# Kernel optimization log

Measured on AMD Instinct MI355X. Metric: run time of the kernel, lower is better.

## Reference

```python
import jax, jax.numpy as jnp
import numpy as np

B, T, D = 4, 1024, 1024       # batch, tokens, emb_size
E, K, F_EXP = 8, 2, 1024      # num_expert, num_expert_active, expert_size
NUM_BLOCK = 12


def setup_inputs() -> dict:
    key = jax.random.key(0)
    k_x, k_b, k_r, k_1, k_2 = jax.random.split(key, 5)
    x = jax.random.normal(k_x, (B, T, D), dtype=jnp.float32)
    auxfree_bias = jax.random.normal(k_b, (E,), dtype=jnp.float32) * 0.1
    router_w = jax.random.normal(k_r, (E, D), dtype=jnp.float32) * 0.02
    # GroupedLinear weight{i}: [out_features, in_features], applied as x @ W^T
    w1 = jax.random.normal(k_1, (E, F_EXP, D), dtype=jnp.float32) * 0.02
    w2 = jax.random.normal(k_2, (E, D, F_EXP), dtype=jnp.float32) * (0.02 / np.sqrt(2.0 * NUM_BLOCK))
    return {"x": x, "auxfree_bias": auxfree_bias, "router_w": router_w, "w1": w1, "w2": w2}


def reference(x, auxfree_bias, router_w, w1, w2):
    # --- routing: top-k on bias-adjusted DETACHED logits, gather raw logits ---
    logits = jnp.einsum("btd,ed->bte", x, router_w)              # [B,T,E]
    biased = jax.lax.stop_gradient(logits) + auxfree_bias        # bias only affects selection
    _, idx = jax.lax.top_k(biased, K)                            # [B,T,K] int32
    gathered = jnp.take_along_axis(logits, idx, axis=-1)         # [B,T,K]
    probs = jax.nn.softmax(gathered, axis=-1)                    # [B,T,K]

    # combine weights per expert: sum_k probs_k * 1[idx_k == e]  -> [B,T,E]
    combine = jnp.sum(jax.nn.one_hot(idx, E, dtype=x.dtype) * probs[..., None], axis=2)

    # --- experts: out = sum_e combine_e * (gelu(x W1_e^T) W2_e^T) ---
    # (dense per-expert reference for the dispatch -> grouped GEMM -> combine pipeline;
    #  tokens with combine weight 0 contribute nothing, matching the sparse original)
    out = jnp.zeros_like(x)
    for e in range(E):
        h = jax.nn.gelu(jnp.einsum("btd,fd->btf", x, w1[e]), approximate=False)
        out = out + combine[:, :, e:e + 1] * jnp.einsum("btf,df->btd", h, w2[e])
    return out
```

## Files before the change

### kernel.cpp

```cpp
#include <hip/hip_runtime.h>
#include <hip/hip_bf16.h>

#define D_DIM 1024
#define F_DIM 1024
#define NTOK  4096
#define NEXP  8
#define CAP   4096

typedef __attribute__((ext_vector_type(8))) short bf16x8;
typedef __attribute__((ext_vector_type(4))) float f32x4;
typedef __attribute__((ext_vector_type(8))) unsigned short u16x8;

__device__ __forceinline__ unsigned short f2bf(float f) {
    unsigned int u = __float_as_uint(f);
    u = u + 0x7fffu + ((u >> 16) & 1u);
    return (unsigned short)(u >> 16);
}

__device__ __forceinline__ void async_copy16(void* lds, const void* gsrc) {
    __builtin_amdgcn_global_load_lds(
        (const __attribute__((address_space(1))) unsigned int*)gsrc,
        (__attribute__((address_space(3))) unsigned int*)lds, 16, 0, 0);
}

__global__ __launch_bounds__(256) void cvt_kernel(const float* __restrict__ in,
                                                  unsigned short* __restrict__ out, int n) {
    int i = (blockIdx.x * 256 + threadIdx.x) * 8;
    if (i >= n) return;
    const float4* p = (const float4*)(in + i);
    float4 a = p[0], b = p[1];
    u16x8 r;
    r[0] = f2bf(a.x); r[1] = f2bf(a.y); r[2] = f2bf(a.z); r[3] = f2bf(a.w);
    r[4] = f2bf(b.x); r[5] = f2bf(b.y); r[6] = f2bf(b.z); r[7] = f2bf(b.w);
    *(u16x8*)(out + i) = r;
}

__global__ __launch_bounds__(256) void logits_kernel(
    const float* __restrict__ x, const float* __restrict__ rw,
    float* __restrict__ logits)
{
    const int wave = threadIdx.x >> 6, lane = threadIdx.x & 63;
    const int t = blockIdx.x * 4 + wave;
    double s[NEXP];
    #pragma unroll
    for (int e = 0; e < NEXP; ++e) s[e] = 0.0;
    const float* xp = x + (size_t)t * D_DIM;
    for (int kk = 0; kk < D_DIM; kk += 64) {
        float xv = xp[kk + lane];
        #pragma unroll
        for (int e = 0; e < NEXP; ++e)
            s[e] += (double)xv * (double)rw[e * D_DIM + kk + lane];
    }
    #pragma unroll
    for (int e = 0; e < NEXP; ++e) {
        double v = s[e];
        for (int off = 32; off; off >>= 1) v += __shfl_xor(v, off, 64);
        s[e] = v;
    }
    if (lane == 0) {
        #pragma unroll
        for (int e = 0; e < NEXP; ++e) logits[(size_t)t * NEXP + e] = (float)s[e];
    }
}

__global__ __launch_bounds__(256) void assign_kernel(
    const float* __restrict__ logits, const float* __restrict__ bias,
    int* counts, int* list, float* wlist)
{
    __shared__ int lcnt[NEXP];
    __shared__ int lbase[NEXP];
    const int tid = threadIdx.x;
    const int t = blockIdx.x * 256 + tid;
    if (tid < NEXP) lcnt[tid] = 0;
    __syncthreads();

    float lg[NEXP], b2[NEXP];
    #pragma unroll
    for (int e = 0; e < NEXP; ++e) {
        lg[e] = logits[(size_t)t * NEXP + e];
        b2[e] = lg[e] + bias[e];
    }
    int i0 = 0; float b0v = b2[0], l0v = lg[0];
    #pragma unroll
    for (int e = 1; e < NEXP; ++e)
        if (b2[e] > b0v) { b0v = b2[e]; l0v = lg[e]; i0 = e; }
    int i1 = -1; float b1v = 0.f, l1v = 0.f;
    #pragma unroll
    for (int e = 0; e < NEXP; ++e) {
        if (e == i0) continue;
        bool take = (i1 < 0) || (b2[e] > b1v);
        if (take) { i1 = e; b1v = b2[e]; l1v = lg[e]; }
    }
    float m = fmaxf(l0v, l1v);
    float e0 = expf(l0v - m), e1 = expf(l1v - m);
    float inv = 1.0f / (e0 + e1);

    int lp0 = atomicAdd(&lcnt[i0], 1);
    int lp1 = atomicAdd(&lcnt[i1], 1);
    __syncthreads();
    if (tid < NEXP) lbase[tid] = atomicAdd(&counts[tid], lcnt[tid]);
    __syncthreads();

    int p0 = lbase[i0] + lp0;
    list[i0 * CAP + p0] = t; wlist[i0 * CAP + p0] = e0 * inv;
    int p1 = lbase[i1] + lp1;
    list[i1 * CAP + p1] = t; wlist[i1 * CAP + p1] = e1 * inv;
}

__global__ void scan_kernel(const int* __restrict__ counts, int* __restrict__ offs) {
    if (threadIdx.x == 0) {
        int a = 0;
        for (int e = 0; e < NEXP; ++e) { offs[e] = a; a += counts[e]; }
        offs[NEXP] = a;
    }
}

#define STAGE(AB, BB, k0)                                                   \
    do {                                                                    \
        _Pragma("unroll")                                                   \
        for (int i = 0; i < 4; ++i) {                                       \
            async_copy16(&AB[(wave * 4 + i) * 512], ap[i] + (k0));          \
            async_copy16(&BB[(wave * 4 + i) * 512], bp_[i] + (k0));         \
        }                                                                   \
    } while (0)

#define COMPUTE(AB, BB)                                                     \
    do {                                                                    \
        _Pragma("unroll")                                                   \
        for (int kk = 0; kk < 2; ++kk) {                                    \
            bf16x8 af[4], bfv[4];                                           \
            const int sbase = kk * 4 + (lane >> 4);                         \
            const int phys  = (sbase ^ (lane & 7)) * 8;                     \
            _Pragma("unroll")                                               \
            for (int m = 0; m < 4; ++m)                                     \
                af[m] = *(const bf16x8*)&AB[(wr * 64 + m * 16 + (lane & 15)) * 64 + phys]; \
            _Pragma("unroll")                                               \
            for (int n = 0; n < 4; ++n)                                     \
                bfv[n] = *(const bf16x8*)&BB[(wc * 64 + n * 16 + (lane & 15)) * 64 + phys]; \
            _Pragma("unroll")                                               \
            for (int m = 0; m < 4; ++m)                                     \
                _Pragma("unroll")                                           \
                for (int n = 0; n < 4; ++n)                                 \
                    acc[m][n] = __builtin_amdgcn_mfma_f32_16x16x32_bf16(af[m], bfv[n], acc[m][n], 0, 0, 0); \
        }                                                                   \
    } while (0)

__global__ __launch_bounds__(256) void gemm1_kernel(
    const unsigned short* __restrict__ xb,
    const unsigned short* __restrict__ w1b,
    const int* __restrict__ counts, const int* __restrict__ offs,
    const int* __restrict__ list,
    unsigned short* __restrict__ H)
{
    const int e  = blockIdx.y >> 5;
    const int rb = blockIdx.y & 31;
    const int ne = counts[e];
    if (rb * 128 >= ne) return;
    const int row0 = rb * 128;
    const int n0 = blockIdx.x * 128;
    const int hbase = offs[e];

    __shared__ __align__(16) unsigned short As0[128 * 64], As1[128 * 64];
    __shared__ __align__(16) unsigned short Bs0[128 * 64], Bs1[128 * 64];
    __shared__ int toks[128];

    const int tid = threadIdx.x;
    if (tid < 128) {
        int i = row0 + tid;
        if (i >= ne) i = ne - 1;
        toks[tid] = list[e * CAP + i];
    }
    __syncthreads();

    const int wave = tid >> 6, lane = tid & 63;
    const int wr = wave >> 1, wc = wave & 1;

    const int lr  = lane >> 3;
    const int swz = ((lane & 7) ^ lr) * 8;
    const unsigned short* ap[4];
    const unsigned short* bp_[4];
    const unsigned short* wbase = w1b + (size_t)e * F_DIM * D_DIM;
    #pragma unroll
    for (int i = 0; i < 4; ++i) {
        int r = wave * 32 + i * 8 + lr;
        ap[i]  = xb + (size_t)toks[r] * D_DIM + swz;
        bp_[i] = wbase + (size_t)(n0 + r) * D_DIM + swz;
    }

    f32x4 acc[4][4];
    #pragma unroll
    for (int m = 0; m < 4; ++m)
        #pragma unroll
        for (int n = 0; n < 4; ++n) acc[m][n] = (f32x4){0.f, 0.f, 0.f, 0.f};

    STAGE(As0, Bs0, 0);
    __syncthreads();
    for (int t = 0; t < 7; ++t) {
        STAGE(As1, Bs1, t * 128 + 64);
        COMPUTE(As0, Bs0);
        __syncthreads();
        STAGE(As0, Bs0, t * 128 + 128);
        COMPUTE(As1, Bs1);
        __syncthreads();
    }
    STAGE(As1, Bs1, 960);
    COMPUTE(As0, Bs0);
    __syncthreads();
    COMPUTE(As1, Bs1);

    #pragma unroll
    for (int m = 0; m < 4; ++m) {
        #pragma unroll
        for (int j = 0; j < 4; ++j) {
            int ri = wr * 64 + m * 16 + (lane >> 4) * 4 + j;
            int i = row0 + ri;
            if (i < ne) {
                unsigned short* hp = H + (size_t)(hbase + i) * F_DIM + n0 + wc * 64;
                #pragma unroll
                for (int n = 0; n < 4; ++n) {
                    float v = acc[m][n][j];
                    float g = 0.5f * v * (1.0f + erff(v * 0.70710678118654752f));
                    hp[n * 16 + (lane & 15)] = f2bf(g);
                }
            }
        }
    }
}

__global__ __launch_bounds__(256) void gemm2_kernel(
    const unsigned short* __restrict__ H,
    const unsigned short* __restrict__ w2b,
    const int* __restrict__ counts, const int* __restrict__ offs,
    const int* __restrict__ list, const float* __restrict__ wlist,
    float* __restrict__ out)
{
    const int e  = blockIdx.y >> 5;
    const int rb = blockIdx.y & 31;
    const int ne = counts[e];
    if (rb * 128 >= ne) return;
    const int row0 = rb * 128;
    const int n0 = blockIdx.x * 128;
    const int hbase = offs[e];

    __shared__ __align__(16) unsigned short As0[128 * 64], As1[128 * 64];
    __shared__ __align__(16) unsigned short Bs0[128 * 64], Bs1[128 * 64];
    __shared__ int toks[128];
    __shared__ float wts[128];

    const int tid = threadIdx.x;
    if (tid < 128) {
        int i = row0 + tid;
        if (i >= ne) i = ne - 1;
        toks[tid] = list[e * CAP + i];
        wts[tid]  = wlist[e * CAP + i];
    }
    __syncthreads();

    const int wave = tid >> 6, lane = tid & 63;
    const int wr = wave >> 1, wc = wave & 1;

    const int lr  = lane >> 3;
    const int swz = ((lane & 7) ^ lr) * 8;
    const unsigned short* ap[4];
    const unsigned short* bp_[4];
    const unsigned short* wbase = w2b + (size_t)e * D_DIM * F_DIM;
    #pragma unroll
    for (int i = 0; i < 4; ++i) {
        int r = wave * 32 + i * 8 + lr;
        ap[i]  = H + (size_t)(hbase + row0 + r) * F_DIM + swz;
        bp_[i] = wbase + (size_t)(n0 + r) * F_DIM + swz;
    }

    f32x4 acc[4][4];
    #pragma unroll
    for (int m = 0; m < 4; ++m)
        #pragma unroll
        for (int n = 0; n < 4; ++n) acc[m][n] = (f32x4){0.f, 0.f, 0.f, 0.f};

    STAGE(As0, Bs0, 0);
    __syncthreads();
    for (int t = 0; t < 7; ++t) {
        STAGE(As1, Bs1, t * 128 + 64);
        COMPUTE(As0, Bs0);
        __syncthreads();
        STAGE(As0, Bs0, t * 128 + 128);
        COMPUTE(As1, Bs1);
        __syncthreads();
    }
    STAGE(As1, Bs1, 960);
    COMPUTE(As0, Bs0);
    __syncthreads();
    COMPUTE(As1, Bs1);

    #pragma unroll
    for (int m = 0; m < 4; ++m) {
        #pragma unroll
        for (int j = 0; j < 4; ++j) {
            int ri = wr * 64 + m * 16 + (lane >> 4) * 4 + j;
            int i = row0 + ri;
            if (i < ne) {
                int t = toks[ri];
                float wt = wts[ri];
                float* op = out + (size_t)t * D_DIM + n0 + wc * 64;
                #pragma unroll
                for (int n = 0; n < 4; ++n)
                    atomicAdd(&op[n * 16 + (lane & 15)], wt * acc[m][n][j]);
            }
        }
    }
}

extern "C" void kernel_launch(void* const* d_in, const int* in_sizes, int n_in,
                              void* d_out, int out_size, void* d_ws, size_t ws_size,
                              hipStream_t stream)
{
    const float* x    = (const float*)d_in[0];
    const float* bias = (const float*)d_in[1];
    const float* rw   = (const float*)d_in[2];
    const float* w1   = (const float*)d_in[3];
    const float* w2   = (const float*)d_in[4];
    float* out = (float*)d_out;

    char* ws = (char*)d_ws;
    size_t cur = 0;
    auto alloc = [&](size_t bytes) -> void* {
        void* p = (void*)(ws + cur);
        cur += (bytes + 255) & ~(size_t)255;
        return p;
    };
    unsigned short* xb   = (unsigned short*)alloc((size_t)NTOK * D_DIM * 2);
    unsigned short* w1b  = (unsigned short*)alloc((size_t)NEXP * F_DIM * D_DIM * 2);
    unsigned short* w2b  = (unsigned short*)alloc((size_t)NEXP * F_DIM * D_DIM * 2);
    unsigned short* Hb   = (unsigned short*)alloc((size_t)(NTOK * 2 + 128) * F_DIM * 2);
    float* logits = (float*)alloc((size_t)NTOK * NEXP * 4);
    int*   list   = (int*)alloc(NEXP * CAP * 4);
    float* wlist  = (float*)alloc(NEXP * CAP * 4);
    int*   counts = (int*)alloc(64);
    int*   offs   = (int*)alloc(64);

    hipMemsetAsync(counts, 0, 64, stream);
    hipMemsetAsync(out, 0, (size_t)out_size * 4, stream);

    cvt_kernel<<<NTOK * D_DIM / 2048, 256, 0, stream>>>(x, xb, NTOK * D_DIM);
    cvt_kernel<<<NEXP * F_DIM * D_DIM / 2048, 256, 0, stream>>>(w1, w1b, NEXP * F_DIM * D_DIM);
    cvt_kernel<<<NEXP * F_DIM * D_DIM / 2048, 256, 0, stream>>>(w2, w2b, NEXP * F_DIM * D_DIM);
    logits_kernel<<<NTOK / 4, 256, 0, stream>>>(x, rw, logits);
    assign_kernel<<<NTOK / 256, 256, 0, stream>>>(logits, bias, counts, list, wlist);
    scan_kernel<<<1, 64, 0, stream>>>(counts, offs);
    gemm1_kernel<<<dim3(8, 256), 256, 0, stream>>>(xb, w1b, counts, offs, list, Hb);
    gemm2_kernel<<<dim3(8, 256), 256, 0, stream>>>(Hb, w2b, counts, offs, list, wlist, out);
}
```

Measured before the change: 251.3 us.

## Shrink GEMM N-tile to 64, drop LDS double buffering, inline expert offset scan

Both grouped GEMMs now use 128x64 output tiles with a single LDS buffer and a simple load-sync-compute-sync loop, doubling the grid in the N dimension. The separate scan kernel is removed; each block computes its expert's row offset by summing counts directly. The smaller tile and smaller LDS footprint are meant to raise occupancy and block count, and removing the scan saves one launch. In exchange, arithmetic intensity per tile drops, the A-tile (gathered tokens) is re-read twice as often, and global loads no longer overlap with MFMA work.

```diff
diff --git a/kernel.cpp b/kernel.cpp
--- a/kernel.cpp
+++ b/kernel.cpp
@@ -107,40 +107,32 @@
     list[i1 * CAP + p1] = t; wlist[i1 * CAP + p1] = e1 * inv;
 }
 
-__global__ void scan_kernel(const int* __restrict__ counts, int* __restrict__ offs) {
-    if (threadIdx.x == 0) {
-        int a = 0;
-        for (int e = 0; e < NEXP; ++e) { offs[e] = a; a += counts[e]; }
-        offs[NEXP] = a;
-    }
-}
-
 #define STAGE(AB, BB, k0)                                                   \
     do {                                                                    \
         _Pragma("unroll")                                                   \
-        for (int i = 0; i < 4; ++i) {                                       \
+        for (int i = 0; i < 4; ++i)                                         \
             async_copy16(&AB[(wave * 4 + i) * 512], ap[i] + (k0));          \
-            async_copy16(&BB[(wave * 4 + i) * 512], bp_[i] + (k0));         \
-        }                                                                   \
+        _Pragma("unroll")                                                   \
+        for (int i = 0; i < 2; ++i)                                         \
+            async_copy16(&BB[(wave * 2 + i) * 512], bp_[i] + (k0));         \
     } while (0)
 
 #define COMPUTE(AB, BB)                                                     \
     do {                                                                    \
         _Pragma("unroll")                                                   \
         for (int kk = 0; kk < 2; ++kk) {                                    \
-            bf16x8 af[4], bfv[4];                                           \
-            const int sbase = kk * 4 + (lane >> 4);                         \
-            const int phys  = (sbase ^ (lane & 7)) * 8;                     \
+            bf16x8 af[4], bfv[2];                                           \
+            const int phys = (((kk * 4) + (lane >> 4)) ^ (lane & 7)) * 8;   \
             _Pragma("unroll")                                               \
             for (int m = 0; m < 4; ++m)                                     \
                 af[m] = *(const bf16x8*)&AB[(wr * 64 + m * 16 + (lane & 15)) * 64 + phys]; \
             _Pragma("unroll")                                               \
-            for (int n = 0; n < 4; ++n)                                     \
-                bfv[n] = *(const bf16x8*)&BB[(wc * 64 + n * 16 + (lane & 15)) * 64 + phys]; \
+            for (int n = 0; n < 2; ++n)                                     \
+                bfv[n] = *(const bf16x8*)&BB[(wc * 32 + n * 16 + (lane & 15)) * 64 + phys]; \
             _Pragma("unroll")                                               \
             for (int m = 0; m < 4; ++m)                                     \
                 _Pragma("unroll")                                           \
-                for (int n = 0; n < 4; ++n)                                 \
+                for (int n = 0; n < 2; ++n)                                 \
                     acc[m][n] = __builtin_amdgcn_mfma_f32_16x16x32_bf16(af[m], bfv[n], acc[m][n], 0, 0, 0); \
         }                                                                   \
     } while (0)
@@ -148,7 +140,7 @@
 __global__ __launch_bounds__(256) void gemm1_kernel(
     const unsigned short* __restrict__ xb,
     const unsigned short* __restrict__ w1b,
-    const int* __restrict__ counts, const int* __restrict__ offs,
+    const int* __restrict__ counts,
     const int* __restrict__ list,
     unsigned short* __restrict__ H)
 {
@@ -157,11 +149,13 @@
     const int ne = counts[e];
     if (rb * 128 >= ne) return;
     const int row0 = rb * 128;
-    const int n0 = blockIdx.x * 128;
-    const int hbase = offs[e];
-
-    __shared__ __align__(16) unsigned short As0[128 * 64], As1[128 * 64];
-    __shared__ __align__(16) unsigned short Bs0[128 * 64], Bs1[128 * 64];
+    const int n0 = blockIdx.x * 64;
+    int hbase = 0;
+    #pragma unroll
+    for (int ee = 0; ee < NEXP; ++ee) if (ee < e) hbase += counts[ee];
+
+    __shared__ __align__(16) unsigned short As[128 * 64];
+    __shared__ __align__(16) unsigned short Bs[64 * 64];
     __shared__ int toks[128];
 
     const int tid = threadIdx.x;
@@ -178,35 +172,27 @@
     const int lr  = lane >> 3;
     const int swz = ((lane & 7) ^ lr) * 8;
     const unsigned short* ap[4];
-    const unsigned short* bp_[4];
+    const unsigned short* bp_[2];
     const unsigned short* wbase = w1b + (size_t)e * F_DIM * D_DIM;
     #pragma unroll
-    for (int i = 0; i < 4; ++i) {
-        int r = wave * 32 + i * 8 + lr;
-        ap[i]  = xb + (size_t)toks[r] * D_DIM + swz;
-        bp_[i] = wbase + (size_t)(n0 + r) * D_DIM + swz;
-    }
-
-    f32x4 acc[4][4];
+    for (int i = 0; i < 4; ++i)
+        ap[i] = xb + (size_t)toks[wave * 32 + i * 8 + lr] * D_DIM + swz;
+    #pragma unroll
+    for (int i = 0; i < 2; ++i)
+        bp_[i] = wbase + (size_t)(n0 + wave * 16 + i * 8 + lr) * D_DIM + swz;
+
+    f32x4 acc[4][2];
     #pragma unroll
     for (int m = 0; m < 4; ++m)
         #pragma unroll
-        for (int n = 0; n < 4; ++n) acc[m][n] = (f32x4){0.f, 0.f, 0.f, 0.f};
-
-    STAGE(As0, Bs0, 0);
-    __syncthreads();
-    for (int t = 0; t < 7; ++t) {
-        STAGE(As1, Bs1, t * 128 + 64);
-        COMPUTE(As0, Bs0);
+        for (int n = 0; n < 2; ++n) acc[m][n] = (f32x4){0.f, 0.f, 0.f, 0.f};
+
+    for (int k0 = 0; k0 < D_DIM; k0 += 64) {
+        STAGE(As, Bs, k0);
         __syncthreads();
-        STAGE(As0, Bs0, t * 128 + 128);
-        COMPUTE(As1, Bs1);
+        COMPUTE(As, Bs);
         __syncthreads();
     }
-    STAGE(As1, Bs1, 960);
-    COMPUTE(As0, Bs0);
-    __syncthreads();
-    COMPUTE(As1, Bs1);
 
     #pragma unroll
     for (int m = 0; m < 4; ++m) {
@@ -215,9 +201,9 @@
             int ri = wr * 64 + m * 16 + (lane >> 4) * 4 + j;
             int i = row0 + ri;
             if (i < ne) {
-                unsigned short* hp = H + (size_t)(hbase + i) * F_DIM + n0 + wc * 64;
+                unsigned short* hp = H + (size_t)(hbase + i) * F_DIM + n0 + wc * 32;
                 #pragma unroll
-                for (int n = 0; n < 4; ++n) {
+                for (int n = 0; n < 2; ++n) {
                     float v = acc[m][n][j];
                     float g = 0.5f * v * (1.0f + erff(v * 0.70710678118654752f));
                     hp[n * 16 + (lane & 15)] = f2bf(g);
@@ -230,7 +216,7 @@
 __global__ __launch_bounds__(256) void gemm2_kernel(
     const unsigned short* __restrict__ H,
     const unsigned short* __restrict__ w2b,
-    const int* __restrict__ counts, const int* __restrict__ offs,
+    const int* __restrict__ counts,
     const int* __restrict__ list, const float* __restrict__ wlist,
     float* __restrict__ out)
 {
@@ -239,11 +225,13 @@
     const int ne = counts[e];
     if (rb * 128 >= ne) return;
     const int row0 = rb * 128;
-    const int n0 = blockIdx.x * 128;
-    const int hbase = offs[e];
-
-    __shared__ __align__(16) unsigned short As0[128 * 64], As1[128 * 64];
-    __shared__ __align__(16) unsigned short Bs0[128 * 64], Bs1[128 * 64];
+    const int n0 = blockIdx.x * 64;
+    int hbase = 0;
+    #pragma unroll
+    for (int ee = 0; ee < NEXP; ++ee) if (ee < e) hbase += counts[ee];
+
+    __shared__ __align__(16) unsigned short As[128 * 64];
+    __shared__ __align__(16) unsigned short Bs[64 * 64];
     __shared__ int toks[128];
     __shared__ float wts[128];
 
@@ -262,35 +250,27 @@
     const int lr  = lane >> 3;
     const int swz = ((lane & 7) ^ lr) * 8;
     const unsigned short* ap[4];
-    const unsigned short* bp_[4];
+    const unsigned short* bp_[2];
     const unsigned short* wbase = w2b + (size_t)e * D_DIM * F_DIM;
     #pragma unroll
-    for (int i = 0; i < 4; ++i) {
-        int r = wave * 32 + i * 8 + lr;
-        ap[i]  = H + (size_t)(hbase + row0 + r) * F_DIM + swz;
-        bp_[i] = wbase + (size_t)(n0 + r) * F_DIM + swz;
-    }
-
-    f32x4 acc[4][4];
+    for (int i = 0; i < 4; ++i)
+        ap[i] = H + (size_t)(hbase + row0 + wave * 32 + i * 8 + lr) * F_DIM + swz;
+    #pragma unroll
+    for (int i = 0; i < 2; ++i)
+        bp_[i] = wbase + (size_t)(n0 + wave * 16 + i * 8 + lr) * F_DIM + swz;
+
+    f32x4 acc[4][2];
     #pragma unroll
     for (int m = 0; m < 4; ++m)
         #pragma unroll
-        for (int n = 0; n < 4; ++n) acc[m][n] = (f32x4){0.f, 0.f, 0.f, 0.f};
-
-    STAGE(As0, Bs0, 0);
-    __syncthreads();
-    for (int t = 0; t < 7; ++t) {
-        STAGE(As1, Bs1, t * 128 + 64);
-        COMPUTE(As0, Bs0);
+        for (int n = 0; n < 2; ++n) acc[m][n] = (f32x4){0.f, 0.f, 0.f, 0.f};
+
+    for (int k0 = 0; k0 < F_DIM; k0 += 64) {
+        STAGE(As, Bs, k0);
         __syncthreads();
-        STAGE(As0, Bs0, t * 128 + 128);
-        COMPUTE(As1, Bs1);
+        COMPUTE(As, Bs);
         __syncthreads();
     }
-    STAGE(As1, Bs1, 960);
-    COMPUTE(As0, Bs0);
-    __syncthreads();
-    COMPUTE(As1, Bs1);
 
     #pragma unroll
     for (int m = 0; m < 4; ++m) {
@@ -301,9 +281,9 @@
             if (i < ne) {
                 int t = toks[ri];
                 float wt = wts[ri];
-                float* op = out + (size_t)t * D_DIM + n0 + wc * 64;
+                float* op = out + (size_t)t * D_DIM + n0 + wc * 32;
                 #pragma unroll
-                for (int n = 0; n < 4; ++n)
+                for (int n = 0; n < 2; ++n)
                     atomicAdd(&op[n * 16 + (lane & 15)], wt * acc[m][n][j]);
             }
         }
@@ -336,7 +316,6 @@
     int*   list   = (int*)alloc(NEXP * CAP * 4);
     float* wlist  = (float*)alloc(NEXP * CAP * 4);
     int*   counts = (int*)alloc(64);
-    int*   offs   = (int*)alloc(64);
 
     hipMemsetAsync(counts, 0, 64, stream);
     hipMemsetAsync(out, 0, (size_t)out_size * 4, stream);
@@ -346,7 +325,6 @@
     cvt_kernel<<<NEXP * F_DIM * D_DIM / 2048, 256, 0, stream>>>(w2, w2b, NEXP * F_DIM * D_DIM);
     logits_kernel<<<NTOK / 4, 256, 0, stream>>>(x, rw, logits);
     assign_kernel<<<NTOK / 256, 256, 0, stream>>>(logits, bias, counts, list, wlist);
-    scan_kernel<<<1, 64, 0, stream>>>(counts, offs);
-    gemm1_kernel<<<dim3(8, 256), 256, 0, stream>>>(xb, w1b, counts, offs, list, Hb);
-    gemm2_kernel<<<dim3(8, 256), 256, 0, stream>>>(Hb, w2b, counts, offs, list, wlist, out);
-}
+    gemm1_kernel<<<dim3(16, 256), 256, 0, stream>>>(xb, w1b, counts, list, Hb);
+    gemm2_kernel<<<dim3(16, 256), 256, 0, stream>>>(Hb, w2b, counts, list, wlist, out);
+}
```

New measurement: 236.5 us. -5.9%, faster.

## Deepen GEMM K-loop prefetch with vmcnt waits and drop scan kernel

Applied to the files above, without the earlier changes.

Replaces the double-buffered K loop in both grouped GEMMs with a fully unrolled loop that keeps two stages in flight. It uses explicit s_waitcnt vmcnt and raw s_barrier instead of __syncthreads, so the async LDS loads for the next tile overlap with compute on the current one. It also removes the single-thread scan kernel launch and computes each expert's row offset inline from the counts. The manual vmcnt counting depends on the exact number of outstanding loads per stage, so a miscount could race.

```diff
diff --git a/kernel.cpp b/kernel.cpp
--- a/kernel.cpp
+++ b/kernel.cpp
@@ -107,14 +107,6 @@
     list[i1 * CAP + p1] = t; wlist[i1 * CAP + p1] = e1 * inv;
 }
 
-__global__ void scan_kernel(const int* __restrict__ counts, int* __restrict__ offs) {
-    if (threadIdx.x == 0) {
-        int a = 0;
-        for (int e = 0; e < NEXP; ++e) { offs[e] = a; a += counts[e]; }
-        offs[NEXP] = a;
-    }
-}
-
 #define STAGE(AB, BB, k0)                                                   \
     do {                                                                    \
         _Pragma("unroll")                                                   \
@@ -129,8 +121,7 @@
         _Pragma("unroll")                                                   \
         for (int kk = 0; kk < 2; ++kk) {                                    \
             bf16x8 af[4], bfv[4];                                           \
-            const int sbase = kk * 4 + (lane >> 4);                         \
-            const int phys  = (sbase ^ (lane & 7)) * 8;                     \
+            const int phys = (((kk * 4) + (lane >> 4)) ^ (lane & 7)) * 8;   \
             _Pragma("unroll")                                               \
             for (int m = 0; m < 4; ++m)                                     \
                 af[m] = *(const bf16x8*)&AB[(wr * 64 + m * 16 + (lane & 15)) * 64 + phys]; \
@@ -145,10 +136,29 @@
         }                                                                   \
     } while (0)
 
+#define KLOOP()                                                             \
+    do {                                                                    \
+        STAGE(As0, Bs0, 0);                                                 \
+        STAGE(As1, Bs1, 64);                                                \
+        _Pragma("unroll")                                                   \
+        for (int t = 0; t < 16; ++t) {                                      \
+            if (t < 15) asm volatile("s_waitcnt vmcnt(8)" ::: "memory");    \
+            else        asm volatile("s_waitcnt vmcnt(0)" ::: "memory");    \
+            __builtin_amdgcn_s_barrier();                                   \
+            if ((t & 1) == 0) COMPUTE(As0, Bs0);                            \
+            else              COMPUTE(As1, Bs1);                            \
+            __builtin_amdgcn_s_barrier();                                   \
+            if (t + 2 < 16) {                                               \
+                if ((t & 1) == 0) STAGE(As0, Bs0, (t + 2) * 64);            \
+                else              STAGE(As1, Bs1, (t + 2) * 64);            \
+            }                                                               \
+        }                                                                   \
+    } while (0)
+
 __global__ __launch_bounds__(256) void gemm1_kernel(
     const unsigned short* __restrict__ xb,
     const unsigned short* __restrict__ w1b,
-    const int* __restrict__ counts, const int* __restrict__ offs,
+    const int* __restrict__ counts,
     const int* __restrict__ list,
     unsigned short* __restrict__ H)
 {
@@ -158,7 +168,9 @@
     if (rb * 128 >= ne) return;
     const int row0 = rb * 128;
     const int n0 = blockIdx.x * 128;
-    const int hbase = offs[e];
+    int hbase = 0;
+    #pragma unroll
+    for (int ee = 0; ee < NEXP; ++ee) if (ee < e) hbase += counts[ee];
 
     __shared__ __align__(16) unsigned short As0[128 * 64], As1[128 * 64];
     __shared__ __align__(16) unsigned short Bs0[128 * 64], Bs1[128 * 64];
@@ -193,20 +205,7 @@
         #pragma unroll
         for (int n = 0; n < 4; ++n) acc[m][n] = (f32x4){0.f, 0.f, 0.f, 0.f};
 
-    STAGE(As0, Bs0, 0);
-    __syncthreads();
-    for (int t = 0; t < 7; ++t) {
-        STAGE(As1, Bs1, t * 128 + 64);
-        COMPUTE(As0, Bs0);
-        __syncthreads();
-        STAGE(As0, Bs0, t * 128 + 128);
-        COMPUTE(As1, Bs1);
-        __syncthreads();
-    }
-    STAGE(As1, Bs1, 960);
-    COMPUTE(As0, Bs0);
-    __syncthreads();
-    COMPUTE(As1, Bs1);
+    KLOOP();
 
     #pragma unroll
     for (int m = 0; m < 4; ++m) {
@@ -230,7 +229,7 @@
 __global__ __launch_bounds__(256) void gemm2_kernel(
     const unsigned short* __restrict__ H,
     const unsigned short* __restrict__ w2b,
-    const int* __restrict__ counts, const int* __restrict__ offs,
+    const int* __restrict__ counts,
     const int* __restrict__ list, const float* __restrict__ wlist,
     float* __restrict__ out)
 {
@@ -240,7 +239,9 @@
     if (rb * 128 >= ne) return;
     const int row0 = rb * 128;
     const int n0 = blockIdx.x * 128;
-    const int hbase = offs[e];
+    int hbase = 0;
+    #pragma unroll
+    for (int ee = 0; ee < NEXP; ++ee) if (ee < e) hbase += counts[ee];
 
     __shared__ __align__(16) unsigned short As0[128 * 64], As1[128 * 64];
     __shared__ __align__(16) unsigned short Bs0[128 * 64], Bs1[128 * 64];
@@ -277,20 +278,7 @@
         #pragma unroll
         for (int n = 0; n < 4; ++n) acc[m][n] = (f32x4){0.f, 0.f, 0.f, 0.f};
 
-    STAGE(As0, Bs0, 0);
-    __syncthreads();
-    for (int t = 0; t < 7; ++t) {
-        STAGE(As1, Bs1, t * 128 + 64);
-        COMPUTE(As0, Bs0);
-        __syncthreads();
-        STAGE(As0, Bs0, t * 128 + 128);
-        COMPUTE(As1, Bs1);
-        __syncthreads();
-    }
-    STAGE(As1, Bs1, 960);
-    COMPUTE(As0, Bs0);
-    __syncthreads();
-    COMPUTE(As1, Bs1);
+    KLOOP();
 
     #pragma unroll
     for (int m = 0; m < 4; ++m) {
@@ -336,7 +324,6 @@
     int*   list   = (int*)alloc(NEXP * CAP * 4);
     float* wlist  = (float*)alloc(NEXP * CAP * 4);
     int*   counts = (int*)alloc(64);
-    int*   offs   = (int*)alloc(64);
 
     hipMemsetAsync(counts, 0, 64, stream);
     hipMemsetAsync(out, 0, (size_t)out_size * 4, stream);
@@ -346,7 +333,6 @@
     cvt_kernel<<<NEXP * F_DIM * D_DIM / 2048, 256, 0, stream>>>(w2, w2b, NEXP * F_DIM * D_DIM);
     logits_kernel<<<NTOK / 4, 256, 0, stream>>>(x, rw, logits);
     assign_kernel<<<NTOK / 256, 256, 0, stream>>>(logits, bias, counts, list, wlist);
-    scan_kernel<<<1, 64, 0, stream>>>(counts, offs);
-    gemm1_kernel<<<dim3(8, 256), 256, 0, stream>>>(xb, w1b, counts, offs, list, Hb);
-    gemm2_kernel<<<dim3(8, 256), 256, 0, stream>>>(Hb, w2b, counts, offs, list, wlist, out);
-}
+    gemm1_kernel<<<dim3(8, 256), 256, 0, stream>>>(xb, w1b, counts, list, Hb);
+    gemm2_kernel<<<dim3(8, 256), 256, 0, stream>>>(Hb, w2b, counts, list, wlist, out);
+}
```

After: 240.8 us. -4.2%, faster.
